# Kernel optimization log

Measured on AMD Instinct MI355X. Metric: run time of the kernel, lower is better.

The kernel has to match this reference:

```python
import jax, jax.numpy as jnp
import numpy as np

NUM_CLASSES = 512


def setup_inputs() -> dict:
    key = jax.random.key(0)
    k1, k2 = jax.random.split(key)
    support_data = jax.random.normal(k1, (2560, 64, 5, 5), dtype=jnp.float32)
    query_data = jax.random.normal(k2, (8192, 64, 5, 5), dtype=jnp.float32)
    # every class 0..511 appears exactly 5 times (sorted, like unique() ordering)
    support_label = (jnp.arange(2560, dtype=jnp.int32) // 5).astype(jnp.int32)
    return {"support_data": support_data, "query_data": query_data,
            "support_label": support_label}


def reference(support_data, query_data, support_label):
    # embedding_net == identity: embeddings are the raw (N, C, H, W) tensors.
    n_q = query_data.shape[0]
    d = support_data.shape[1] * support_data.shape[2] * support_data.shape[3]
    s = support_data.reshape(support_data.shape[0], d)   # [Ns, d]
    q = query_data.reshape(n_q, d)                        # [Nq, d]

    # class-mean prototypes (scatter-mean == per-unique-label mean loop)
    sums = jax.ops.segment_sum(s, support_label, num_segments=NUM_CLASSES)      # [M, d]
    counts = jax.ops.segment_sum(jnp.ones((s.shape[0],), s.dtype),
                                 support_label, num_segments=NUM_CLASSES)       # [M]
    protos = sums / counts[:, None]                                             # [M, d]

    # squared euclidean distance: ||q||^2 + ||p||^2 - 2 q.p  (same math as
    # broadcast (q - p)**2 summed over c,h,w, without the [Nq,M,d] intermediate)
    q2 = jnp.sum(q * q, axis=1, keepdims=True)            # [Nq, 1]
    p2 = jnp.sum(protos * protos, axis=1)                 # [M]
    dist = q2 + p2[None, :] - 2.0 * (q @ protos.T)        # [Nq, M]

    return jax.nn.log_softmax(-dist, axis=1)
```

## Files before the change

kernel.cpp:

```cpp
#include <hip/hip_runtime.h>
#include <hip/hip_bf16.h>
#include <cstdint>
#include <cstddef>

#define NS 2560
#define NQ 8192
#define NC 512
#define DD 1600

typedef __bf16 bf16_t;
typedef __bf16 bf16x4 __attribute__((ext_vector_type(4)));
typedef __bf16 bf16x8 __attribute__((ext_vector_type(8)));
typedef float f32x4 __attribute__((ext_vector_type(4)));

__global__ __launch_bounds__(256) void proto_kernel(
    const float* __restrict__ sup, const int* __restrict__ lab,
    bf16_t* __restrict__ protos, float* __restrict__ p2)
{
    const int m   = blockIdx.x;
    const int tid = threadIdx.x;
    __shared__ int   idxs[32];
    __shared__ int   cnt;
    __shared__ float wsum[4];
    if (tid == 0) cnt = 0;
    __syncthreads();
    for (int i = tid; i < NS; i += 256) {
        if (lab[i] == m) {
            int p = atomicAdd(&cnt, 1);
            if (p < 32) idxs[p] = i;
        }
    }
    __syncthreads();
    int n = cnt < 32 ? cnt : 32;
    if (tid == 0 && n > 1) {
        for (int a = 1; a < n; ++a) {
            int key = idxs[a]; int b = a - 1;
            while (b >= 0 && idxs[b] > key) { idxs[b+1] = idxs[b]; --b; }
            idxs[b+1] = key;
        }
    }
    __syncthreads();

    float acc[7];
    #pragma unroll
    for (int u = 0; u < 7; ++u) acc[u] = 0.f;
    for (int t = 0; t < n; ++t) {
        const float* src = sup + (size_t)idxs[t] * DD;
        #pragma unroll
        for (int u = 0; u < 7; ++u) {
            int j = tid + u * 256;
            if (j < DD) acc[u] += src[j];
        }
    }
    float inv = (n > 0) ? 1.f / (float)n : 0.f;
    float psq = 0.f;
    #pragma unroll
    for (int u = 0; u < 7; ++u) {
        int j = tid + u * 256;
        if (j < DD) {
            float p = acc[u] * inv;
            bf16_t pb = (bf16_t)p;
            protos[(size_t)m * DD + j] = pb;
            float pf = (float)pb;
            psq += pf * pf;
        }
    }
    #pragma unroll
    for (int o = 32; o > 0; o >>= 1) psq += __shfl_xor(psq, o);
    int lane = tid & 63, wid = tid >> 6;
    if (lane == 0) wsum[wid] = psq;
    __syncthreads();
    if (tid == 0) p2[m] = wsum[0] + wsum[1] + wsum[2] + wsum[3];
}

__device__ __forceinline__ void stage_B_wave(const bf16_t* __restrict__ protos,
                                             char* strip, int k0, int lane, int wid)
{
    #pragma unroll
    for (int p = 0; p < 8; ++p) {
        int gidx = p * 64 + lane;
        int row  = gidx >> 3;
        int gcol = gidx & 7;
        const bf16_t* src = protos + (size_t)(wid * 64 + row) * DD + k0
                          + ((gcol ^ (row & 7)) * 8);
        char* dst = strip + p * 1024;
        __builtin_amdgcn_global_load_lds(
            (const __attribute__((address_space(1))) void*)src,
            (__attribute__((address_space(3))) void*)dst, 16, 0, 0);
    }
}

__global__ __launch_bounds__(512, 2) void fused_kernel(
    const float* __restrict__ q, const bf16_t* __restrict__ protos,
    const float* __restrict__ p2, float* __restrict__ out)
{
    extern __shared__ char smem[];

    const int tid  = threadIdx.x;
    const int lane = tid & 63;
    const int wid  = tid >> 6;
    const int r    = lane & 15;
    const int g    = lane >> 4;
    const int m0   = blockIdx.x * 32;

    float p2c[4];
    #pragma unroll
    for (int ni = 0; ni < 4; ++ni) p2c[ni] = p2[wid * 64 + ni * 16 + r];

    f32x4 acc[2][4];
    #pragma unroll
    for (int mi = 0; mi < 2; ++mi)
        #pragma unroll
        for (int ni = 0; ni < 4; ++ni)
            acc[mi][ni] = (f32x4){0.f, 0.f, 0.f, 0.f};

    const int arow = tid >> 4;
    const int acg  = tid & 15;
    const float* aptr = q + (size_t)(m0 + arow) * DD + acg * 4;
    const int    aoff = (arow * 128 + acg * 8) ^ ((arow & 7) << 4);

    {
        float4 f = *(const float4*)(aptr);
        __builtin_amdgcn_sched_barrier(0);
        stage_B_wave(protos, smem + wid * 8192, 0, lane, wid);
        __builtin_amdgcn_sched_barrier(0);
        bf16x4 w;
        w[0] = (bf16_t)f.x; w[1] = (bf16_t)f.y; w[2] = (bf16_t)f.z; w[3] = (bf16_t)f.w;
        *(bf16x4*)(smem + 131072 + aoff) = w;
        asm volatile("s_waitcnt lgkmcnt(0)" ::: "memory");
        __builtin_amdgcn_sched_barrier(0);
        __builtin_amdgcn_s_barrier();
        __builtin_amdgcn_sched_barrier(0);
    }

    for (int t = 0; t < 25; ++t) {
        const int cur = t & 1;
        const char* bstrip  = smem + cur * 65536 + wid * 8192;
        char*       bstripn = smem + (cur ^ 1) * 65536 + wid * 8192;
        const char* as      = smem + 131072 + cur * 4096;
        char*       asn     = smem + 131072 + (cur ^ 1) * 4096;
        const bool  pre     = (t < 24);

        float4 fA;
        if (pre) fA = *(const float4*)(aptr + (t + 1) * 64);
        __builtin_amdgcn_sched_barrier(0);
        if (pre) stage_B_wave(protos, bstripn, (t + 1) * 64, lane, wid);
        __builtin_amdgcn_sched_barrier(0);

        if (pre) asm volatile("s_waitcnt vmcnt(9)" ::: "memory");
        else     asm volatile("s_waitcnt vmcnt(0)" ::: "memory");
        __builtin_amdgcn_sched_barrier(0);

        #pragma unroll
        for (int kk = 0; kk < 2; ++kk) {
            bf16x8 af[2], bfr[4];
            #pragma unroll
            for (int mi = 0; mi < 2; ++mi) {
                int ab = ((mi * 16 + r) * 128 + kk * 64 + g * 16) ^ ((r & 7) << 4);
                af[mi] = *(const bf16x8*)(as + ab);
            }
            #pragma unroll
            for (int ni = 0; ni < 4; ++ni) {
                int c  = ni * 16 + r;
                int bb = (c * 128 + kk * 64 + g * 16) ^ ((c & 7) << 4);
                bfr[ni] = *(const bf16x8*)(bstrip + bb);
            }
            #pragma unroll
            for (int mi = 0; mi < 2; ++mi)
                #pragma unroll
                for (int ni = 0; ni < 4; ++ni)
                    acc[mi][ni] = __builtin_amdgcn_mfma_f32_16x16x32_bf16(
                        af[mi], bfr[ni], acc[mi][ni], 0, 0, 0);
        }

        if (pre) {
            bf16x4 w;
            w[0] = (bf16_t)fA.x; w[1] = (bf16_t)fA.y;
            w[2] = (bf16_t)fA.z; w[3] = (bf16_t)fA.w;
            *(bf16x4*)(asn + aoff) = w;
        }
        asm volatile("s_waitcnt lgkmcnt(0)" ::: "memory");
        __builtin_amdgcn_sched_barrier(0);
        __builtin_amdgcn_s_barrier();
        __builtin_amdgcn_sched_barrier(0);
    }

    #pragma unroll
    for (int mi = 0; mi < 2; ++mi)
        #pragma unroll
        for (int ni = 0; ni < 4; ++ni)
            #pragma unroll
            for (int j = 0; j < 4; ++j)
                acc[mi][ni][j] = 2.f * acc[mi][ni][j] - p2c[ni];

    float* red  = (float*)smem;
    float* gmax = red + 256;
    float* lse  = gmax + 32;

    float rmax[2][4];
    #pragma unroll
    for (int mi = 0; mi < 2; ++mi)
        #pragma unroll
        for (int j = 0; j < 4; ++j) {
            float m = acc[mi][0][j];
            #pragma unroll
            for (int ni = 1; ni < 4; ++ni) m = fmaxf(m, acc[mi][ni][j]);
            rmax[mi][j] = m;
        }
    #pragma unroll
    for (int o = 1; o < 16; o <<= 1)
        #pragma unroll
        for (int mi = 0; mi < 2; ++mi)
            #pragma unroll
            for (int j = 0; j < 4; ++j)
                rmax[mi][j] = fmaxf(rmax[mi][j], __shfl_xor(rmax[mi][j], o));
    if (r == 0) {
        #pragma unroll
        for (int mi = 0; mi < 2; ++mi)
            #pragma unroll
            for (int j = 0; j < 4; ++j)
                red[(mi * 16 + g * 4 + j) * 8 + wid] = rmax[mi][j];
    }
    __syncthreads();
    if (tid < 32) {
        float m = red[tid * 8];
        #pragma unroll
        for (int w = 1; w < 8; ++w) m = fmaxf(m, red[tid * 8 + w]);
        gmax[tid] = m;
    }
    __syncthreads();

    float rsum[2][4];
    #pragma unroll
    for (int mi = 0; mi < 2; ++mi)
        #pragma unroll
        for (int j = 0; j < 4; ++j) {
            float gm = gmax[mi * 16 + g * 4 + j];
            float s = 0.f;
            #pragma unroll
            for (int ni = 0; ni < 4; ++ni) s += expf(acc[mi][ni][j] - gm);
            rsum[mi][j] = s;
        }
    #pragma unroll
    for (int o = 1; o < 16; o <<= 1)
        #pragma unroll
        for (int mi = 0; mi < 2; ++mi)
            #pragma unroll
            for (int j = 0; j < 4; ++j)
                rsum[mi][j] += __shfl_xor(rsum[mi][j], o);
    if (r == 0) {
        #pragma unroll
        for (int mi = 0; mi < 2; ++mi)
            #pragma unroll
            for (int j = 0; j < 4; ++j)
                red[(mi * 16 + g * 4 + j) * 8 + wid] = rsum[mi][j];
    }
    __syncthreads();
    if (tid < 32) {
        float s = 0.f;
        #pragma unroll
        for (int w = 0; w < 8; ++w) s += red[tid * 8 + w];
        lse[tid] = gmax[tid] + logf(s);
    }
    __syncthreads();

    #pragma unroll
    for (int mi = 0; mi < 2; ++mi) {
        #pragma unroll
        for (int j = 0; j < 4; ++j) {
            float l = lse[mi * 16 + g * 4 + j];
            size_t rowoff = (size_t)(m0 + mi * 16 + g * 4 + j) * NC;
            #pragma unroll
            for (int ni = 0; ni < 4; ++ni)
                out[rowoff + wid * 64 + ni * 16 + r] = acc[mi][ni][j] - l;
        }
    }
}

extern "C" void kernel_launch(void* const* d_in, const int* in_sizes, int n_in,
                              void* d_out, int out_size, void* d_ws, size_t ws_size,
                              hipStream_t stream)
{
    const float* sup = (const float*)d_in[0];
    const float* qry = (const float*)d_in[1];
    const int*   lab = (const int*)d_in[2];
    float* out = (float*)d_out;

    char* ws = (char*)d_ws;
    bf16_t* protos = (bf16_t*)ws;
    float*  p2     = (float*)(ws + 1638400);

    const int smem_bytes = 139264;
    hipFuncSetAttribute(reinterpret_cast<const void*>(fused_kernel),
                        hipFuncAttributeMaxDynamicSharedMemorySize, smem_bytes);

    proto_kernel<<<NC, 256, 0, stream>>>(sup, lab, protos, p2);
    fused_kernel<<<NQ / 32, 512, smem_bytes, stream>>>(qry, protos, p2, out);
}
```

Baseline: 60.71 us.

## Load prototype B fragments directly into registers instead of staging through LDS

Each wave now reads its prototype MFMA operands straight from global memory into registers, double-buffered across k-steps. The 128KB LDS B staging via global_load_lds and the dynamic shared memory setup are removed. LDS use drops to a few KB for the A tile and reductions, which frees LDS and may allow more blocks per CU. In exchange, register pressure rises (16 bf16x8 buffers), and global loads are less coalesced, with each lane reading 16B chunks from separate rows.

```diff
diff --git a/kernel.cpp b/kernel.cpp
--- a/kernel.cpp
+++ b/kernel.cpp
@@ -73,28 +73,63 @@
     if (tid == 0) p2[m] = wsum[0] + wsum[1] + wsum[2] + wsum[3];
 }
 
-__device__ __forceinline__ void stage_B_wave(const bf16_t* __restrict__ protos,
-                                             char* strip, int k0, int lane, int wid)
-{
-    #pragma unroll
-    for (int p = 0; p < 8; ++p) {
-        int gidx = p * 64 + lane;
-        int row  = gidx >> 3;
-        int gcol = gidx & 7;
-        const bf16_t* src = protos + (size_t)(wid * 64 + row) * DD + k0
-                          + ((gcol ^ (row & 7)) * 8);
-        char* dst = strip + p * 1024;
-        __builtin_amdgcn_global_load_lds(
-            (const __attribute__((address_space(1))) void*)src,
-            (__attribute__((address_space(3))) void*)dst, 16, 0, 0);
-    }
+__device__ __forceinline__ void gemm_body(
+    bf16x8 (&BC)[8], bf16x8 (&BN)[8], const char* ACUR, char* ANXT,
+    int T, const char* bbase, const float* aptr, int aoff,
+    int r, int g, f32x4 (&acc)[2][4])
+{
+    const int  Tn  = T + 1;
+    const bool pre = (Tn < 25);
+
+    float4 fA;
+    if (pre) {
+        fA = *(const float4*)(aptr + Tn * 64);
+        #pragma unroll
+        for (int ni = 0; ni < 4; ++ni)
+            #pragma unroll
+            for (int kk = 0; kk < 2; ++kk)
+                BN[ni * 2 + kk] = *(const bf16x8*)(bbase
+                    + ni * (16 * 2 * DD) + Tn * 128 + kk * 64);
+    }
+    __builtin_amdgcn_sched_barrier(0);
+
+    bf16x8 af[2][2];
+    #pragma unroll
+    for (int kk = 0; kk < 2; ++kk)
+        #pragma unroll
+        for (int mi = 0; mi < 2; ++mi)
+            af[kk][mi] = *(const bf16x8*)(ACUR +
+                ((((mi * 16 + r) * 128) + kk * 64 + g * 16) ^ ((r & 7) << 4)));
+
+    #pragma unroll
+    for (int kk = 0; kk < 2; ++kk)
+        #pragma unroll
+        for (int mi = 0; mi < 2; ++mi)
+            #pragma unroll
+            for (int ni = 0; ni < 4; ++ni)
+                acc[mi][ni] = __builtin_amdgcn_mfma_f32_16x16x32_bf16(
+                    af[kk][mi], BC[ni * 2 + kk], acc[mi][ni], 0, 0, 0);
+
+    if (pre) {
+        bf16x4 w;
+        w[0] = (bf16_t)fA.x; w[1] = (bf16_t)fA.y;
+        w[2] = (bf16_t)fA.z; w[3] = (bf16_t)fA.w;
+        *(bf16x4*)(ANXT + aoff) = w;
+    }
+    asm volatile("s_waitcnt lgkmcnt(0)" ::: "memory");
+    __builtin_amdgcn_sched_barrier(0);
+    __builtin_amdgcn_s_barrier();
+    __builtin_amdgcn_sched_barrier(0);
 }
 
 __global__ __launch_bounds__(512, 2) void fused_kernel(
     const float* __restrict__ q, const bf16_t* __restrict__ protos,
     const float* __restrict__ p2, float* __restrict__ out)
 {
-    extern __shared__ char smem[];
+    __shared__ char  Asm[2][4096];
+    __shared__ float red[32 * 8];
+    __shared__ float gmaxs[32];
+    __shared__ float lses[32];
 
     const int tid  = threadIdx.x;
     const int lane = tid & 63;
@@ -103,6 +138,8 @@
     const int g    = lane >> 4;
     const int m0   = blockIdx.x * 32;
 
+    const char* bbase = (const char*)protos + (size_t)(wid * 64 + r) * (2 * DD) + g * 16;
+
     float p2c[4];
     #pragma unroll
     for (int ni = 0; ni < 4; ++ni) p2c[ni] = p2[wid * 64 + ni * 16 + r];
@@ -119,71 +156,32 @@
     const float* aptr = q + (size_t)(m0 + arow) * DD + acg * 4;
     const int    aoff = (arow * 128 + acg * 8) ^ ((arow & 7) << 4);
 
+    bf16x8 b0[8], b1[8];
+
     {
         float4 f = *(const float4*)(aptr);
         __builtin_amdgcn_sched_barrier(0);
-        stage_B_wave(protos, smem + wid * 8192, 0, lane, wid);
+        #pragma unroll
+        for (int ni = 0; ni < 4; ++ni)
+            #pragma unroll
+            for (int kk = 0; kk < 2; ++kk)
+                b0[ni * 2 + kk] = *(const bf16x8*)(bbase
+                    + ni * (16 * 2 * DD) + kk * 64);
         __builtin_amdgcn_sched_barrier(0);
         bf16x4 w;
         w[0] = (bf16_t)f.x; w[1] = (bf16_t)f.y; w[2] = (bf16_t)f.z; w[3] = (bf16_t)f.w;
-        *(bf16x4*)(smem + 131072 + aoff) = w;
+        *(bf16x4*)(&Asm[0][0] + aoff) = w;
         asm volatile("s_waitcnt lgkmcnt(0)" ::: "memory");
         __builtin_amdgcn_sched_barrier(0);
         __builtin_amdgcn_s_barrier();
         __builtin_amdgcn_sched_barrier(0);
     }
 
-    for (int t = 0; t < 25; ++t) {
-        const int cur = t & 1;
-        const char* bstrip  = smem + cur * 65536 + wid * 8192;
-        char*       bstripn = smem + (cur ^ 1) * 65536 + wid * 8192;
-        const char* as      = smem + 131072 + cur * 4096;
-        char*       asn     = smem + 131072 + (cur ^ 1) * 4096;
-        const bool  pre     = (t < 24);
-
-        float4 fA;
-        if (pre) fA = *(const float4*)(aptr + (t + 1) * 64);
-        __builtin_amdgcn_sched_barrier(0);
-        if (pre) stage_B_wave(protos, bstripn, (t + 1) * 64, lane, wid);
-        __builtin_amdgcn_sched_barrier(0);
-
-        if (pre) asm volatile("s_waitcnt vmcnt(9)" ::: "memory");
-        else     asm volatile("s_waitcnt vmcnt(0)" ::: "memory");
-        __builtin_amdgcn_sched_barrier(0);
-
-        #pragma unroll
-        for (int kk = 0; kk < 2; ++kk) {
-            bf16x8 af[2], bfr[4];
-            #pragma unroll
-            for (int mi = 0; mi < 2; ++mi) {
-                int ab = ((mi * 16 + r) * 128 + kk * 64 + g * 16) ^ ((r & 7) << 4);
-                af[mi] = *(const bf16x8*)(as + ab);
-            }
-            #pragma unroll
-            for (int ni = 0; ni < 4; ++ni) {
-                int c  = ni * 16 + r;
-                int bb = (c * 128 + kk * 64 + g * 16) ^ ((c & 7) << 4);
-                bfr[ni] = *(const bf16x8*)(bstrip + bb);
-            }
-            #pragma unroll
-            for (int mi = 0; mi < 2; ++mi)
-                #pragma unroll
-                for (int ni = 0; ni < 4; ++ni)
-                    acc[mi][ni] = __builtin_amdgcn_mfma_f32_16x16x32_bf16(
-                        af[mi], bfr[ni], acc[mi][ni], 0, 0, 0);
-        }
-
-        if (pre) {
-            bf16x4 w;
-            w[0] = (bf16_t)fA.x; w[1] = (bf16_t)fA.y;
-            w[2] = (bf16_t)fA.z; w[3] = (bf16_t)fA.w;
-            *(bf16x4*)(asn + aoff) = w;
-        }
-        asm volatile("s_waitcnt lgkmcnt(0)" ::: "memory");
-        __builtin_amdgcn_sched_barrier(0);
-        __builtin_amdgcn_s_barrier();
-        __builtin_amdgcn_sched_barrier(0);
-    }
+    for (int tt = 0; tt < 24; tt += 2) {
+        gemm_body(b0, b1, &Asm[0][0], &Asm[1][0], tt,     bbase, aptr, aoff, r, g, acc);
+        gemm_body(b1, b0, &Asm[1][0], &Asm[0][0], tt + 1, bbase, aptr, aoff, r, g, acc);
+    }
+    gemm_body(b0, b1, &Asm[0][0], &Asm[1][0], 24, bbase, aptr, aoff, r, g, acc);
 
     #pragma unroll
     for (int mi = 0; mi < 2; ++mi)
@@ -192,10 +190,6 @@
             #pragma unroll
             for (int j = 0; j < 4; ++j)
                 acc[mi][ni][j] = 2.f * acc[mi][ni][j] - p2c[ni];
-
-    float* red  = (float*)smem;
-    float* gmax = red + 256;
-    float* lse  = gmax + 32;
 
     float rmax[2][4];
     #pragma unroll
@@ -226,7 +220,7 @@
         float m = red[tid * 8];
         #pragma unroll
         for (int w = 1; w < 8; ++w) m = fmaxf(m, red[tid * 8 + w]);
-        gmax[tid] = m;
+        gmaxs[tid] = m;
     }
     __syncthreads();
 
@@ -235,7 +229,7 @@
     for (int mi = 0; mi < 2; ++mi)
         #pragma unroll
         for (int j = 0; j < 4; ++j) {
-            float gm = gmax[mi * 16 + g * 4 + j];
+            float gm = gmaxs[mi * 16 + g * 4 + j];
             float s = 0.f;
             #pragma unroll
             for (int ni = 0; ni < 4; ++ni) s += expf(acc[mi][ni][j] - gm);
@@ -260,7 +254,7 @@
         float s = 0.f;
         #pragma unroll
         for (int w = 0; w < 8; ++w) s += red[tid * 8 + w];
-        lse[tid] = gmax[tid] + logf(s);
+        lses[tid] = gmaxs[tid] + logf(s);
     }
     __syncthreads();
 
@@ -268,7 +262,7 @@
     for (int mi = 0; mi < 2; ++mi) {
         #pragma unroll
         for (int j = 0; j < 4; ++j) {
-            float l = lse[mi * 16 + g * 4 + j];
+            float l = lses[mi * 16 + g * 4 + j];
             size_t rowoff = (size_t)(m0 + mi * 16 + g * 4 + j) * NC;
             #pragma unroll
             for (int ni = 0; ni < 4; ++ni)
@@ -290,10 +284,6 @@
     bf16_t* protos = (bf16_t*)ws;
     float*  p2     = (float*)(ws + 1638400);
 
-    const int smem_bytes = 139264;
-    hipFuncSetAttribute(reinterpret_cast<const void*>(fused_kernel),
-                        hipFuncAttributeMaxDynamicSharedMemorySize, smem_bytes);
-
     proto_kernel<<<NC, 256, 0, stream>>>(sup, lab, protos, p2);
-    fused_kernel<<<NQ / 32, 512, smem_bytes, stream>>>(qry, protos, p2, out);
-}
+    fused_kernel<<<NQ / 32, 512, 0, stream>>>(qry, protos, p2, out);
+}
```

Result: slower. 76.44 us (+25.9%).
